# Optimization experiments

Measured on AMD Instinct MI355X. Metric: run time of the kernel, lower is better.

Reference implementation:

```python
import jax, jax.numpy as jnp
import numpy as np

B, IN, OUT, LAT, HID = 65536, 1, 512, 128, 2048
COEFFS = (IN + 1) * OUT * 2  # (in+1)*out*n_harmonics*n_eig = 2048

def setup_inputs() -> dict:
    key = jax.random.key(0)
    k = jax.random.split(key, 6)
    x = jax.random.normal(k[0], (B, IN + 1 + LAT), dtype=jnp.float32)
    fc1_w = jax.random.normal(k[1], (LAT, HID), dtype=jnp.float32) * (1.0 / np.sqrt(LAT))
    fc1_b = jax.random.normal(k[2], (HID,), dtype=jnp.float32) * 0.02
    fc2_w = jax.random.normal(k[3], (HID, COEFFS), dtype=jnp.float32) * (1.0 / np.sqrt(HID))
    fc2_b = jax.random.normal(k[4], (COEFFS,), dtype=jnp.float32) * 0.02
    dil = jnp.ones((4,), dtype=jnp.float32)      # dilation1..4
    shift_p = jnp.zeros((4,), dtype=jnp.float32)  # shift1..4
    return {"x": x, "fc1_w": fc1_w, "fc1_b": fc1_b, "fc2_w": fc2_w,
            "fc2_b": fc2_b, "dil": dil, "shift_p": shift_p}

def reference(x, fc1_w, fc1_b, fc2_w, fc2_b, dil, shift_p):
    s = x[-1, IN]                       # scalar time of last sample
    inp = x[:, :IN]                     # [B, 1]
    z = x[:, -LAT:]                     # [B, LAT]
    # CoeffDecoder: tanh MLP
    h = jnp.tanh(z @ fc1_w + fc1_b)     # [B, HID]
    coeffs = (h @ fc2_w + fc2_b).reshape(B, (IN + 1) * OUT, 2)
    # aew trig basis Bin (2x4) has only 4 nonzeros; X.sum(2) == coeffs @ Bin.sum(axis=1)
    t = s * dil + shift_p               # [4]
    v = jnp.stack([jnp.cos(t[0]) + jnp.cos(t[2]),
                   jnp.sin(t[1]) + jnp.sin(t[3])])  # [2] = row-sums of Bin
    w = coeffs @ v                      # [B, (IN+1)*OUT]
    weight = w[:, :IN * OUT].reshape(B, IN, OUT)
    bias = w[:, IN * OUT:(IN + 1) * OUT]
    weighted = jnp.einsum('bi,bio->bo', inp, weight)  # bmm([B,1,1],[B,1,OUT]).squeeze(1)
    return weighted + bias              # [B, OUT]
```

## Files before the change

### kernel.cpp

```cpp
#include <hip/hip_runtime.h>
#include <hip/hip_bf16.h>
#include <stddef.h>

#define NB   65536
#define XC   130
#define LATD 128
#define HIDD 2048
#define JC   1024
#define OC   512
#define BM   128
#define BN   512

typedef __bf16 bf16_t;
typedef bf16_t bf16x8 __attribute__((ext_vector_type(8)));
typedef float  f32x4  __attribute__((ext_vector_type(4)));

typedef __attribute__((address_space(1))) const unsigned char ga_u8;
typedef __attribute__((address_space(3))) unsigned char ls_u8;

__device__ __forceinline__ void dma16(const void* g, void* l) {
  __builtin_amdgcn_global_load_lds((ga_u8*)g, (ls_u8*)l, 16, 0, 0);
}

__global__ void prep_fc1(const float* __restrict__ fc1w, bf16_t* __restrict__ fc1wT) {
  int t = blockIdx.x * blockDim.x + threadIdx.x;
  int k = t & (LATD - 1);
  int n = t >> 7;
  fc1wT[(size_t)n * LATD + k] = (bf16_t)fc1w[(size_t)k * HIDD + n];
}

__global__ void prep_fc2(const float* __restrict__ x, const float* __restrict__ fc2w,
                         const float* __restrict__ fc2b, const float* __restrict__ dil,
                         const float* __restrict__ shp, bf16_t* __restrict__ w2pT,
                         float* __restrict__ b2p) {
  int t = blockIdx.x * blockDim.x + threadIdx.x;
  int k = t & (HIDD - 1);
  int c = t >> 11;
  float s  = x[(size_t)(NB - 1) * XC + 1];
  float t0 = s * dil[0] + shp[0];
  float t1 = s * dil[1] + shp[1];
  float t2 = s * dil[2] + shp[2];
  float t3 = s * dil[3] + shp[3];
  float v0 = cosf(t0) + cosf(t2);
  float v1 = sinf(t1) + sinf(t3);
  int jj = ((c >> 5) * 16 + (c & 15)) + (((c >> 4) & 1) << 9);
  float w0 = fc2w[(size_t)k * 2048 + 2 * jj];
  float w1 = fc2w[(size_t)k * 2048 + 2 * jj + 1];
  w2pT[(size_t)c * HIDD + k] = (bf16_t)(w0 * v0 + w1 * v1);
  if (k == 0) b2p[c] = fc2b[2 * jj] * v0 + fc2b[2 * jj + 1] * v1;
}

__global__ __launch_bounds__(512, 2) void wag_main(
    const float* __restrict__ x, const float* __restrict__ fc1b,
    const bf16_t* __restrict__ fc1wT, const bf16_t* __restrict__ w2pT,
    const float* __restrict__ b2p, float* __restrict__ out)
{
  __shared__ bf16_t w2t[BN * 64];
  __shared__ bf16_t f1t[2][64 * LATD];
  __shared__ bf16_t h_lds[2][BM * 64];
  __shared__ float  inp_lds[BM];

  const int t   = threadIdx.x;
  const int w   = t >> 6;
  const int l   = t & 63;
  const int lhi = l >> 4;
  const int llo = l & 15;
  const size_t b0 = (size_t)blockIdx.x * BM;
  const int    bc = blockIdx.y * BN;

  bf16x8 za[4];
  {
    const float* zsrc = x + (b0 + w * 16 + llo) * XC + 2;
#pragma unroll
    for (int ks = 0; ks < 4; ++ks) {
      bf16x8 pk;
#pragma unroll
      for (int i = 0; i < 4; ++i) {
        float2 f = *(const float2*)(zsrc + ks * 32 + lhi * 8 + 2 * i);
        pk[2 * i]     = (bf16_t)f.x;
        pk[2 * i + 1] = (bf16_t)f.y;
      }
      za[ks] = pk;
    }
    if (t < BM) inp_lds[t] = x[(b0 + t) * XC];
  }

  f32x4 acc[4][8] = {};

  auto stage_w2 = [&](int kc) {
#pragma unroll
    for (int q = 0; q < 8; ++q) {
      int j   = w * 8 + q;
      int col = j * 8 + (l >> 3);
      int kb  = ((l & 7) * 16) ^ ((col & 7) << 4);
      const char* src = (const char*)w2pT + ((size_t)(bc + col) * HIDD + kc * 64) * 2 + kb;
      dma16(src, (char*)w2t + j * 1024);
    }
  };
  auto stage_f1 = [&](int j64, int buf) {
#pragma unroll
    for (int q = 0; q < 2; ++q) {
      int j   = w * 2 + q;
      int col = j * 4 + (l >> 4);
      int kb  = ((l & 15) * 16) ^ ((col & 7) << 4);
      const char* src = (const char*)fc1wT + ((size_t)(j64 * 64 + col) * LATD) * 2 + kb;
      dma16(src, (char*)f1t[buf] + j * 1024);
    }
  };

  auto G1 = [&](int j) {
    const int buf = j & 1;
#pragma unroll
    for (int nt = 0; nt < 4; ++nt) {
      int col = nt * 16 + llo;
      f32x4 c1 = {};
#pragma unroll
      for (int ks = 0; ks < 4; ++ks) {
        int fb = col * 256 + ((ks * 64 + lhi * 16) ^ ((col & 7) << 4));
        bf16x8 b = *(const bf16x8*)((const char*)f1t[buf] + fb);
        c1 = __builtin_amdgcn_mfma_f32_16x16x32_bf16(za[ks], b, c1, 0, 0, 0);
      }
      float bias = fc1b[j * 64 + col];
#pragma unroll
      for (int r = 0; r < 4; ++r) {
        float pre = c1[r] + bias;
        float e   = __builtin_amdgcn_exp2f(pre * 2.88539008177792681f);
        float th  = 1.0f - 2.0f * __builtin_amdgcn_rcpf(e + 1.0f);
        int hr = w * 16 + lhi * 4 + r;
        int hb = (hr * 128 + col * 2) ^ ((hr & 7) << 4);
        *(bf16_t*)((char*)h_lds[buf] + hb) = (bf16_t)th;
      }
    }
  };

  auto G2 = [&](int kc) {
    const int hbuf = kc & 1;
    const int mrb  = (w & 1) * 64;
    const int ncb  = (w >> 1) * 128;
#pragma unroll
    for (int ks = 0; ks < 2; ++ks) {
      bf16x8 a[4];
#pragma unroll
      for (int mt = 0; mt < 4; ++mt) {
        int hr = mrb + mt * 16 + llo;
        a[mt] = *(const bf16x8*)((const char*)h_lds[hbuf] +
                 ((hr * 128 + ks * 64 + lhi * 16) ^ ((hr & 7) << 4)));
      }
#pragma unroll
      for (int nt = 0; nt < 8; ++nt) {
        int col = ncb + nt * 16 + llo;
        int wb  = col * 128 + ((ks * 64 + lhi * 16) ^ ((col & 7) << 4));
        bf16x8 b = *(const bf16x8*)((const char*)w2t + wb);
#pragma unroll
        for (int mt = 0; mt < 4; ++mt)
          acc[mt][nt] = __builtin_amdgcn_mfma_f32_16x16x32_bf16(a[mt], b, acc[mt][nt], 0, 0, 0);
      }
    }
  };

  stage_f1(0, 0);
  stage_w2(0);
  __syncthreads();
  stage_f1(1, 1);
  G1(0);
  __syncthreads();

  for (int kc = 0; kc < 31; ++kc) {
    G2(kc);
    __syncthreads();
    stage_w2(kc + 1);
    if (kc < 30) stage_f1(kc + 2, kc & 1);
    G1(kc + 1);
    __syncthreads();
  }
  G2(31);

  {
    const int mrb = (w & 1) * 64;
    const int ncb = (w >> 1) * 128;
#pragma unroll
    for (int p = 0; p < 4; ++p) {
      int cw = bc + ncb + p * 32 + llo;
      float bw = b2p[cw];
      float bb = b2p[cw + 16];
      int oc = (bc + ncb + p * 32) / 2 + llo;
#pragma unroll
      for (int mt = 0; mt < 4; ++mt) {
#pragma unroll
        for (int r = 0; r < 4; ++r) {
          int row = mrb + mt * 16 + lhi * 4 + r;
          float wv = acc[mt][2 * p][r] + bw;
          float bv = acc[mt][2 * p + 1][r] + bb;
          out[(b0 + row) * OC + oc] = inp_lds[row] * wv + bv;
        }
      }
    }
  }
}

extern "C" void kernel_launch(void* const* d_in, const int* in_sizes, int n_in,
                              void* d_out, int out_size, void* d_ws, size_t ws_size,
                              hipStream_t stream) {
  const float* x    = (const float*)d_in[0];
  const float* fc1w = (const float*)d_in[1];
  const float* fc1b = (const float*)d_in[2];
  const float* fc2w = (const float*)d_in[3];
  const float* fc2b = (const float*)d_in[4];
  const float* dil  = (const float*)d_in[5];
  const float* shp  = (const float*)d_in[6];
  float* out = (float*)d_out;

  bf16_t* fc1wT = (bf16_t*)d_ws;
  bf16_t* w2pT  = fc1wT + (size_t)HIDD * LATD;
  float*  b2p   = (float*)(w2pT + (size_t)JC * HIDD);

  prep_fc1<<<(HIDD * LATD) / 256, 256, 0, stream>>>(fc1w, fc1wT);
  prep_fc2<<<(JC * HIDD) / 256, 256, 0, stream>>>(x, fc2w, fc2b, dil, shp, w2pT, b2p);
  wag_main<<<dim3(NB / BM, JC / BN), 512, 0, stream>>>(x, fc1b, fc1wT, w2pT, b2p, out);
}
```

Baseline: 514.0 us.

## Halve K chunk, double-buffer W2 tile, and overlap staging with MFMA

The K-chunk drops from 64 to 32 and the fc2 weight tile in LDS becomes double-buffered. Each iteration now issues the next W2/fc1 DMA and the next tanh-GEMM before the current GEMM2, using one barrier per iteration instead of two. The GEMM2 MFMA loop is also wrapped in s_setprio to favour matrix issue. The aim is to hide global-load and G1 latency behind GEMM2. In exchange, the W2 LDS layout loses its XOR swizzle, which may add bank conflicts, and smaller chunks mean more iterations, each with less work to amortise its overhead.

```diff
diff --git a/kernel.cpp b/kernel.cpp
--- a/kernel.cpp
+++ b/kernel.cpp
@@ -10,6 +10,8 @@
 #define OC   512
 #define BM   128
 #define BN   512
+#define KCH  32
+#define NKC  64
 
 typedef __bf16 bf16_t;
 typedef bf16_t bf16x8 __attribute__((ext_vector_type(8)));
@@ -55,9 +57,9 @@
     const bf16_t* __restrict__ fc1wT, const bf16_t* __restrict__ w2pT,
     const float* __restrict__ b2p, float* __restrict__ out)
 {
-  __shared__ bf16_t w2t[BN * 64];
-  __shared__ bf16_t f1t[2][64 * LATD];
-  __shared__ bf16_t h_lds[2][BM * 64];
+  __shared__ bf16_t w2t[2][BN * KCH];
+  __shared__ bf16_t f1t[2][KCH * LATD];
+  __shared__ bf16_t h_lds[BM * 64];
   __shared__ float  inp_lds[BM];
 
   const int t   = threadIdx.x;
@@ -88,30 +90,26 @@
   f32x4 acc[4][8] = {};
 
   auto stage_w2 = [&](int kc) {
-#pragma unroll
-    for (int q = 0; q < 8; ++q) {
-      int j   = w * 8 + q;
-      int col = j * 8 + (l >> 3);
-      int kb  = ((l & 7) * 16) ^ ((col & 7) << 4);
-      const char* src = (const char*)w2pT + ((size_t)(bc + col) * HIDD + kc * 64) * 2 + kb;
-      dma16(src, (char*)w2t + j * 1024);
+    const int buf = kc & 1;
+#pragma unroll
+    for (int q = 0; q < 4; ++q) {
+      int j   = w * 4 + q;
+      int col = j * 16 + (l >> 2);
+      const char* src = (const char*)(w2pT + (size_t)(bc + col) * HIDD + kc * KCH + (l & 3) * 8);
+      dma16(src, (char*)w2t[buf] + j * 1024);
     }
   };
   auto stage_f1 = [&](int j64, int buf) {
-#pragma unroll
-    for (int q = 0; q < 2; ++q) {
-      int j   = w * 2 + q;
-      int col = j * 4 + (l >> 4);
-      int kb  = ((l & 15) * 16) ^ ((col & 7) << 4);
-      const char* src = (const char*)fc1wT + ((size_t)(j64 * 64 + col) * LATD) * 2 + kb;
-      dma16(src, (char*)f1t[buf] + j * 1024);
-    }
+    int col = w * 4 + (l >> 4);
+    int kb  = ((l & 15) * 16) ^ ((col & 7) << 4);
+    const char* src = (const char*)fc1wT + ((size_t)(j64 * KCH + col) * LATD) * 2 + kb;
+    dma16(src, (char*)f1t[buf] + w * 1024);
   };
 
   auto G1 = [&](int j) {
     const int buf = j & 1;
 #pragma unroll
-    for (int nt = 0; nt < 4; ++nt) {
+    for (int nt = 0; nt < 2; ++nt) {
       int col = nt * 16 + llo;
       f32x4 c1 = {};
 #pragma unroll
@@ -120,42 +118,40 @@
         bf16x8 b = *(const bf16x8*)((const char*)f1t[buf] + fb);
         c1 = __builtin_amdgcn_mfma_f32_16x16x32_bf16(za[ks], b, c1, 0, 0, 0);
       }
-      float bias = fc1b[j * 64 + col];
+      float bias = fc1b[j * KCH + col];
 #pragma unroll
       for (int r = 0; r < 4; ++r) {
         float pre = c1[r] + bias;
         float e   = __builtin_amdgcn_exp2f(pre * 2.88539008177792681f);
         float th  = 1.0f - 2.0f * __builtin_amdgcn_rcpf(e + 1.0f);
         int hr = w * 16 + lhi * 4 + r;
-        int hb = (hr * 128 + col * 2) ^ ((hr & 7) << 4);
-        *(bf16_t*)((char*)h_lds[buf] + hb) = (bf16_t)th;
+        int hb = (hr * 128 + (buf * KCH + col) * 2) ^ ((hr & 7) << 4);
+        *(bf16_t*)((char*)h_lds + hb) = (bf16_t)th;
       }
     }
   };
 
   auto G2 = [&](int kc) {
-    const int hbuf = kc & 1;
-    const int mrb  = (w & 1) * 64;
-    const int ncb  = (w >> 1) * 128;
-#pragma unroll
-    for (int ks = 0; ks < 2; ++ks) {
-      bf16x8 a[4];
-#pragma unroll
-      for (int mt = 0; mt < 4; ++mt) {
-        int hr = mrb + mt * 16 + llo;
-        a[mt] = *(const bf16x8*)((const char*)h_lds[hbuf] +
-                 ((hr * 128 + ks * 64 + lhi * 16) ^ ((hr & 7) << 4)));
-      }
-#pragma unroll
-      for (int nt = 0; nt < 8; ++nt) {
-        int col = ncb + nt * 16 + llo;
-        int wb  = col * 128 + ((ks * 64 + lhi * 16) ^ ((col & 7) << 4));
-        bf16x8 b = *(const bf16x8*)((const char*)w2t + wb);
-#pragma unroll
-        for (int mt = 0; mt < 4; ++mt)
-          acc[mt][nt] = __builtin_amdgcn_mfma_f32_16x16x32_bf16(a[mt], b, acc[mt][nt], 0, 0, 0);
-      }
-    }
+    const int buf = kc & 1;
+    const int mrb = (w & 1) * 64;
+    const int ncb = (w >> 1) * 128;
+    bf16x8 a[4];
+#pragma unroll
+    for (int mt = 0; mt < 4; ++mt) {
+      int hr = mrb + mt * 16 + llo;
+      a[mt] = *(const bf16x8*)((const char*)h_lds +
+               (hr * 128 + ((buf * 64 + lhi * 16) ^ ((hr & 7) << 4))));
+    }
+    __builtin_amdgcn_s_setprio(1);
+#pragma unroll
+    for (int nt = 0; nt < 8; ++nt) {
+      int col = ncb + nt * 16 + llo;
+      bf16x8 b = *(const bf16x8*)((const char*)w2t[buf] + (col * 64 + lhi * 16));
+#pragma unroll
+      for (int mt = 0; mt < 4; ++mt)
+        acc[mt][nt] = __builtin_amdgcn_mfma_f32_16x16x32_bf16(a[mt], b, acc[mt][nt], 0, 0, 0);
+    }
+    __builtin_amdgcn_s_setprio(0);
   };
 
   stage_f1(0, 0);
@@ -165,15 +161,13 @@
   G1(0);
   __syncthreads();
 
-  for (int kc = 0; kc < 31; ++kc) {
+  for (int kc = 0; kc < NKC; ++kc) {
+    if (kc < NKC - 1) stage_w2(kc + 1);
+    if (kc < NKC - 2) stage_f1(kc + 2, kc & 1);
+    if (kc < NKC - 1) G1(kc + 1);
     G2(kc);
-    __syncthreads();
-    stage_w2(kc + 1);
-    if (kc < 30) stage_f1(kc + 2, kc & 1);
-    G1(kc + 1);
-    __syncthreads();
+    if (kc < NKC - 1) __syncthreads();
   }
-  G2(31);
 
   {
     const int mrb = (w & 1) * 64;
```

Result: faster. 498.4 us (-3.0%).
